# Optimization experiments

Hardware: AMD Instinct MI355X
Metric: run time of the kernel (lower is better)

The kernel has to match this reference:

```python
import jax, jax.numpy as jnp
import numpy as np

WIDTH = 16
N_LAYERS = 2
N_HIGHWAY = 2
B, S, D = 16, 2048, 512


def _causal_band(x, w):
    # out[:, t] = sum_{d=0..WIDTH} w[WIDTH-d] * x[:, t-d]  (x[<0]=0)
    out = w[WIDTH] * x
    for d in range(1, WIDTH + 1):
        out = out + w[WIDTH - d] * jnp.pad(x, ((0, 0), (d, 0), (0, 0)))[:, :S]
    return out


def _anticausal_band(x, w):
    # out[:, t] = sum_{d=0..WIDTH} w[d] * x[:, t+d]  (x[>=S]=0)
    out = w[0] * x
    for d in range(1, WIDTH + 1):
        out = out + w[d] * jnp.pad(x, ((0, 0), (0, d), (0, 0)))[:, d:]
    return out


def _highway(x, Ws, bs):
    # Ws: [N_HIGHWAY, D, 2D], bs: [N_HIGHWAY, 2D] (allennlp Highway, relu activation)
    for i in range(N_HIGHWAY):
        proj = jnp.einsum('bsd,de->bse', x, Ws[i]) + bs[i]
        nonlinear, gate = jnp.split(proj, 2, axis=-1)
        g = jax.nn.sigmoid(gate)
        x = g * x + (1.0 - g) * jax.nn.relu(nonlinear)
    return x


def setup_inputs() -> dict:
    key = jax.random.key(0)
    ks = jax.random.split(key, 8)
    scale = 1.0 / np.sqrt(D)
    return {
        'inputs': jax.random.normal(ks[0], (B, S, D), jnp.float32),
        'masks': jnp.ones((B, S), jnp.int32),
        'fw_band': jax.random.normal(ks[1], (N_LAYERS, WIDTH + 1), jnp.float32),
        'bw_band': jax.random.normal(ks[2], (N_LAYERS, WIDTH + 1), jnp.float32),
        'fw_W': jax.random.normal(ks[3], (N_LAYERS, N_HIGHWAY, D, 2 * D), jnp.float32) * scale,
        'fw_b': jax.random.normal(ks[4], (N_LAYERS, N_HIGHWAY, 2 * D), jnp.float32) * 0.1,
        'bw_W': jax.random.normal(ks[5], (N_LAYERS, N_HIGHWAY, D, 2 * D), jnp.float32) * scale,
        'bw_b': jax.random.normal(ks[6], (N_LAYERS, N_HIGHWAY, 2 * D), jnp.float32) * 0.1,
    }


def reference(inputs, masks, fw_band, bw_band, fw_W, fw_b, bw_W, bw_b):
    fwd = inputs
    bwd = inputs
    outs = []
    for l in range(N_LAYERS):
        fwd = _causal_band(fwd, fw_band[l])
        bwd = _anticausal_band(bwd, bw_band[l])
        fwd = _highway(fwd, fw_W[l], fw_b[l])
        bwd = _highway(bwd, bw_W[l], bw_b[l])
        outs.append(jnp.concatenate([fwd, bwd], axis=-1))
    return jnp.stack(outs, axis=0)  # [N_LAYERS, B, S, 2D]
```

## Files before the change

### kernel.cpp

```cpp
#include <hip/hip_runtime.h>
#include <hip/hip_bf16.h>

#define B_ 16
#define S_ 2048
#define D_ 512
#define M_ (B_ * S_)

typedef __attribute__((ext_vector_type(8))) _Float16 f16x8;
typedef __attribute__((ext_vector_type(4))) float f32x4;

#define GLOAD_LDS16(gp, lp)                                                   \
    __builtin_amdgcn_global_load_lds(                                         \
        (const __attribute__((address_space(1))) unsigned int*)(gp),          \
        (__attribute__((address_space(3))) unsigned int*)(lp), 16, 0, 0)

__global__ __launch_bounds__(256) void prep_w_kernel(
    const float* __restrict__ fwW, const float* __restrict__ bwW,
    _Float16* __restrict__ Wt)
{
    __shared__ float tile[32][33];
    int bid = blockIdx.x;
    int mat = bid >> 9;
    int t   = bid & 511;
    int kt  = t >> 5;
    int nt  = t & 31;
    int l   = mat >> 2;
    int dir = (mat >> 1) & 1;
    int h   = mat & 1;
    const float* src = (dir ? bwW : fwW) + (long long)(l * 2 + h) * (512LL * 1024);

    int tx = threadIdx.x & 31;
    int ty = threadIdx.x >> 5;
#pragma unroll
    for (int j = 0; j < 4; ++j) {
        int k = kt * 32 + ty + j * 8;
        tile[ty + j * 8][tx] = src[(long long)k * 1024 + nt * 32 + tx];
    }
    __syncthreads();
    _Float16* dst = Wt + (long long)mat * (1024LL * 512);
#pragma unroll
    for (int j = 0; j < 4; ++j) {
        int n = nt * 32 + ty + j * 8;
        dst[(long long)n * 512 + kt * 32 + tx] = (_Float16)tile[tx][ty + j * 8];
    }
}

__global__ __launch_bounds__(256) void band_conv_kernel(
    const float* __restrict__ src, long long bstride, int rstride,
    const float* __restrict__ w17, int causal,
    _Float16* __restrict__ Th)
{
    int id = blockIdx.x * 256 + threadIdx.x;
    int c  = id & (D_ - 1);
    int tt = (id >> 9) & (S_ / 4 - 1);
    int b  = id >> 18;
    int t0 = tt * 4;

    float w[17];
#pragma unroll
    for (int e = 0; e < 17; ++e) w[e] = w17[e];

    float buf[20];
    int tbase = t0 - (causal ? 16 : 0);
    const float* sp = src + (long long)b * bstride + c;
#pragma unroll
    for (int i = 0; i < 20; ++i) {
        int t = tbase + i;
        buf[i] = (t >= 0 && t < S_) ? sp[(long long)t * rstride] : 0.f;
    }
#pragma unroll
    for (int j = 0; j < 4; ++j) {
        float a = 0.f;
#pragma unroll
        for (int e = 0; e <= 16; ++e) a = fmaf(w[e], buf[j + e], a);
        Th[((long long)(b * S_ + t0 + j)) * D_ + c] = (_Float16)a;
    }
}

__global__ __launch_bounds__(256) void hw_step_kernel(
    const _Float16* __restrict__ Xh,
    const _Float16* __restrict__ Wt,
    const float* __restrict__ bias,
    float* __restrict__ outF, int outF_stride,
    _Float16* __restrict__ outH)
{
    __shared__ _Float16 As[2 * 128 * 32];
    __shared__ _Float16 Bs[2 * 128 * 32];

    int tid = threadIdx.x;

    int f = blockIdx.x;
    int L = (f & 7) * 256 + (f >> 3);
    int colb = L & 7;
    int rowb = L >> 3;
    long long m0 = (long long)rowb * 128;
    int n0   = colb * 64;

    int lane = tid & 63;
    int wave = tid >> 6;
    int wm   = (wave & 1) * 64;
    int wn   = (wave >> 1) * 32;
    int ln   = lane & 15;
    int q    = lane >> 4;

    f32x4 acc[2][2][4];
#pragma unroll
    for (int h = 0; h < 2; ++h)
#pragma unroll
        for (int jn = 0; jn < 2; ++jn)
#pragma unroll
            for (int i = 0; i < 4; ++i) acc[h][jn][i] = (f32x4){0.f, 0.f, 0.f, 0.f};

    int srow = tid >> 2;
    int scol = (tid & 3) * 8;
    const _Float16* gA0 = Xh + (m0 + srow) * 512 + scol;
    const _Float16* gA1 = gA0 + 64 * 512;
    const _Float16* gB0 = Wt + (long long)(n0 + srow) * 512 + scol;
    const _Float16* gB1 = gB0 + 512 * 512;

    auto stage = [&](int b, int k0) {
        _Float16* lA = &As[b * 4096 + tid * 8];
        _Float16* lB = &Bs[b * 4096 + tid * 8];
        GLOAD_LDS16(gA0 + k0, lA);
        GLOAD_LDS16(gA1 + k0, lA + 64 * 32);
        GLOAD_LDS16(gB0 + k0, lB);
        GLOAD_LDS16(gB1 + k0, lB + 64 * 32);
    };

    auto compute = [&](int b) {
        const _Float16* Ab = &As[b * 4096];
        const _Float16* Bb = &Bs[b * 4096];
        f16x8 af[4];
#pragma unroll
        for (int i = 0; i < 4; ++i)
            af[i] = *(const f16x8*)&Ab[(wm + i * 16 + ln) * 32 + q * 8];
        f16x8 bfr[2][2];
#pragma unroll
        for (int h = 0; h < 2; ++h)
#pragma unroll
            for (int jn = 0; jn < 2; ++jn)
                bfr[h][jn] = *(const f16x8*)&Bb[(h * 64 + wn + jn * 16 + ln) * 32 + q * 8];
#pragma unroll
        for (int h = 0; h < 2; ++h)
#pragma unroll
            for (int jn = 0; jn < 2; ++jn)
#pragma unroll
                for (int i = 0; i < 4; ++i)
                    acc[h][jn][i] = __builtin_amdgcn_mfma_f32_16x16x32_f16(
                        af[i], bfr[h][jn], acc[h][jn][i], 0, 0, 0);
    };

    stage(0, 0);
    __syncthreads();
    int cur = 0;
    for (int k0 = 32; k0 < 512; k0 += 32) {
        stage(cur ^ 1, k0);
        compute(cur);
        __syncthreads();
        cur ^= 1;
    }
    compute(cur);

    __syncthreads();
    {
        int xrow = tid >> 3;
        int xcol = (tid & 7) * 8;
        const _Float16* gx = Xh + (m0 + xrow) * 512 + n0 + xcol;
#pragma unroll
        for (int j = 0; j < 4; ++j)
            GLOAD_LDS16(gx + (long long)j * 32 * 512, &As[j * 2048 + tid * 8]);
    }
    __syncthreads();

#pragma unroll
    for (int jn = 0; jn < 2; ++jn) {
        int c  = n0 + wn + jn * 16 + ln;
        int xc = wn + jn * 16 + ln;
        float bnl = bias[c];
        float bg  = bias[512 + c];
#pragma unroll
        for (int i = 0; i < 4; ++i) {
#pragma unroll
            for (int r = 0; r < 4; ++r) {
                int xr = wm + i * 16 + q * 4 + r;
                long long m = m0 + xr;
                float nl = acc[0][jn][i][r] + bnl;
                float gt = acc[1][jn][i][r] + bg;
                float g  = 1.f / (1.f + __expf(-gt));
                float xv = (float)As[xr * 64 + xc];
                float o  = g * xv + (1.f - g) * fmaxf(nl, 0.f);
                if (outF) outF[m * (long long)outF_stride + c] = o;
                if (outH) outH[m * 512 + c] = (_Float16)o;
            }
        }
    }
}

extern "C" void kernel_launch(void* const* d_in, const int* in_sizes, int n_in,
                              void* d_out, int out_size, void* d_ws, size_t ws_size,
                              hipStream_t stream)
{
    const float* inputs  = (const float*)d_in[0];
    const float* fw_band = (const float*)d_in[2];
    const float* bw_band = (const float*)d_in[3];
    const float* fw_W    = (const float*)d_in[4];
    const float* fw_b    = (const float*)d_in[5];
    const float* bw_W    = (const float*)d_in[6];
    const float* bw_b    = (const float*)d_in[7];
    float* out = (float*)d_out;

    char* ws = (char*)d_ws;
    const size_t SZ_TH = (size_t)M_ * D_ * 2;
    _Float16* Th = (_Float16*)(ws);
    _Float16* Hh = (_Float16*)(ws + SZ_TH);
    _Float16* Wt = (_Float16*)(ws + 2 * SZ_TH);

    prep_w_kernel<<<4096, 256, 0, stream>>>(fw_W, bw_W, Wt);

    for (int l = 0; l < 2; ++l) {
        for (int dir = 0; dir < 2; ++dir) {
            const float* src; long long bstride; int rstride;
            if (l == 0) { src = inputs; bstride = (long long)S_ * D_; rstride = D_; }
            else {
                src = out + (long long)(l - 1) * M_ * 1024 + dir * 512;
                bstride = (long long)S_ * 1024; rstride = 1024;
            }
            const float* band = (dir ? bw_band : fw_band) + l * 17;
            band_conv_kernel<<<(B_ * (S_ / 4) * D_) / 256, 256, 0, stream>>>(
                src, bstride, rstride, band, dir == 0 ? 1 : 0, Th);

            const _Float16* W0 = Wt + (size_t)((l * 2 + dir) * 2 + 0) * (1024 * 512);
            const _Float16* W1 = Wt + (size_t)((l * 2 + dir) * 2 + 1) * (1024 * 512);
            const float* bias = (dir ? bw_b : fw_b) + (size_t)(l * 2) * 1024;

            hw_step_kernel<<<2048, 256, 0, stream>>>(Th, W0, bias, nullptr, 0, Hh);
            float* oF = out + (long long)l * M_ * 1024 + dir * 512;
            hw_step_kernel<<<2048, 256, 0, stream>>>(Hh, W1, bias + 1024, oF, 1024, nullptr);
        }
    }
}
```

Measured before the change: 892.1 us.

## Enlarge highway GEMM tile with swizzled LDS and fine-grained staged pipeline

The highway GEMM kernel moves from a 128x64 output tile (times two for gate and nonlinear halves) with K-step 32 to a 256x128 tile with K-step 64, using 512 threads and a 128KB LDS double buffer. LDS rows get an XOR swizzle to avoid bank conflicts. Global-to-LDS loads are split into per-phase stages interleaved with the MFMA blocks, using explicit vmcnt waits, barriers and s_setprio. The aim is more operand reuse per byte loaded and better overlap of loads with math, at the cost of much higher LDS use, roughly one block per CU, and tricky manual synchronisation.

Result: faster. 821.3 us (-7.9%).

```diff
diff --git a/kernel.cpp b/kernel.cpp
--- a/kernel.cpp
+++ b/kernel.cpp
@@ -77,117 +77,141 @@
     }
 }
 
-__global__ __launch_bounds__(256) void hw_step_kernel(
+__global__ __launch_bounds__(512, 2) void hw_step_kernel(
     const _Float16* __restrict__ Xh,
     const _Float16* __restrict__ Wt,
     const float* __restrict__ bias,
     float* __restrict__ outF, int outF_stride,
     _Float16* __restrict__ outH)
 {
-    __shared__ _Float16 As[2 * 128 * 32];
-    __shared__ _Float16 Bs[2 * 128 * 32];
+    __shared__ _Float16 lds[65536];
+    char* ldsb = (char*)lds;
 
     int tid = threadIdx.x;
 
     int f = blockIdx.x;
-    int L = (f & 7) * 256 + (f >> 3);
-    int colb = L & 7;
-    int rowb = L >> 3;
-    long long m0 = (long long)rowb * 128;
-    int n0   = colb * 64;
+    int L = (f & 7) * 64 + (f >> 3);
+    int colb = L & 3;
+    int rowb = L >> 2;
+    long long m0 = (long long)rowb * 256;
+    int n0 = colb * 128;
 
     int lane = tid & 63;
     int wave = tid >> 6;
-    int wm   = (wave & 1) * 64;
-    int wn   = (wave >> 1) * 32;
-    int ln   = lane & 15;
-    int q    = lane >> 4;
-
-    f32x4 acc[2][2][4];
+    int wave_m = wave >> 1;
+    int wave_n = wave & 1;
+    int wrow = wave_m * 64;
+    int wn   = wave_n * 64;
+    int ln = lane & 15;
+    int q  = lane >> 4;
+
+    int rloc  = tid >> 3;
+    int cperm = 8 * ((tid & 7) ^ (rloc & 7));
+    const _Float16* gA  = Xh + (m0 + rloc) * 512 + cperm;
+    const _Float16* gBn = Wt + (long long)(n0 + rloc) * 512 + cperm;
+    const _Float16* gBg = Wt + (long long)(512 + n0 + rloc) * 512 + cperm;
+
+    auto stageA = [&](int b, int kt, int h2) {
+#pragma unroll
+        for (int j = 0; j < 2; ++j)
+            GLOAD_LDS16(gA + (long long)(h2 * 128 + j * 64) * 512 + kt * 64,
+                        ldsb + b * 32768 + h2 * 16384 + (j * 512 + tid) * 16);
+    };
+    auto stageB = [&](int b, int kt, int h2) {
+        const _Float16* g = h2 ? gBg : gBn;
+#pragma unroll
+        for (int j = 0; j < 2; ++j)
+            GLOAD_LDS16(g + (long long)(j * 64) * 512 + kt * 64,
+                        ldsb + 65536 + b * 32768 + h2 * 16384 + (j * 512 + tid) * 16);
+    };
+
+    f32x4 acc[2][4][4];
 #pragma unroll
     for (int h = 0; h < 2; ++h)
 #pragma unroll
-        for (int jn = 0; jn < 2; ++jn)
+        for (int jn = 0; jn < 4; ++jn)
 #pragma unroll
             for (int i = 0; i < 4; ++i) acc[h][jn][i] = (f32x4){0.f, 0.f, 0.f, 0.f};
 
-    int srow = tid >> 2;
-    int scol = (tid & 3) * 8;
-    const _Float16* gA0 = Xh + (m0 + srow) * 512 + scol;
-    const _Float16* gA1 = gA0 + 64 * 512;
-    const _Float16* gB0 = Wt + (long long)(n0 + srow) * 512 + scol;
-    const _Float16* gB1 = gB0 + 512 * 512;
-
-    auto stage = [&](int b, int k0) {
-        _Float16* lA = &As[b * 4096 + tid * 8];
-        _Float16* lB = &Bs[b * 4096 + tid * 8];
-        GLOAD_LDS16(gA0 + k0, lA);
-        GLOAD_LDS16(gA1 + k0, lA + 64 * 32);
-        GLOAD_LDS16(gB0 + k0, lB);
-        GLOAD_LDS16(gB1 + k0, lB + 64 * 32);
-    };
-
-    auto compute = [&](int b) {
-        const _Float16* Ab = &As[b * 4096];
-        const _Float16* Bb = &Bs[b * 4096];
-        f16x8 af[4];
-#pragma unroll
-        for (int i = 0; i < 4; ++i)
-            af[i] = *(const f16x8*)&Ab[(wm + i * 16 + ln) * 32 + q * 8];
-        f16x8 bfr[2][2];
-#pragma unroll
-        for (int h = 0; h < 2; ++h)
-#pragma unroll
-            for (int jn = 0; jn < 2; ++jn)
-                bfr[h][jn] = *(const f16x8*)&Bb[(h * 64 + wn + jn * 16 + ln) * 32 + q * 8];
-#pragma unroll
-        for (int h = 0; h < 2; ++h)
-#pragma unroll
-            for (int jn = 0; jn < 2; ++jn)
+    stageB(0, 0, 0);
+    stageA(0, 0, 0);
+    stageA(0, 0, 1);
+    stageB(0, 0, 1);
+    stageB(1, 1, 0);
+    asm volatile("s_waitcnt vmcnt(2)" ::: "memory");
+    __builtin_amdgcn_s_barrier();
+
+    f16x8 af[4];
+    for (int kt = 0; kt < 8; ++kt) {
+        int b = kt & 1;
+        const char* Ab = ldsb + b * 32768;
+        const char* Bb = ldsb + 65536 + b * 32768;
+#pragma unroll
+        for (int p = 0; p < 4; ++p) {
+            const int h = p & 1, ks = p >> 1;
+            const int cb = ks * 64 + q * 16;
+            if ((p & 1) == 0) {
+#pragma unroll
+                for (int i = 0; i < 4; ++i) {
+                    int row = wrow + i * 16 + ln;
+                    af[i] = *(const f16x8*)(Ab + row * 128 + (cb ^ ((row & 7) << 4)));
+                }
+            }
+            f16x8 bf[4];
+#pragma unroll
+            for (int jn = 0; jn < 4; ++jn) {
+                int row = h * 128 + wn + jn * 16 + ln;
+                bf[jn] = *(const f16x8*)(Bb + row * 128 + (cb ^ ((row & 7) << 4)));
+            }
+            if (p == 0) { if (kt + 1 < 8) stageA(b ^ 1, kt + 1, 0); }
+            if (p == 1) { if (kt + 1 < 8) stageA(b ^ 1, kt + 1, 1); }
+            if (p == 2) { if (kt + 1 < 8) stageB(b ^ 1, kt + 1, 1); }
+            if (p == 3) {
+                if (kt + 2 < 8) stageB(b, kt + 2, 0);
+                if (kt < 6)       asm volatile("s_waitcnt vmcnt(2)" ::: "memory");
+                else if (kt == 6) asm volatile("s_waitcnt vmcnt(0)" ::: "memory");
+            }
+            __builtin_amdgcn_s_barrier();
+            asm volatile("s_waitcnt lgkmcnt(0)" ::: "memory");
+            __builtin_amdgcn_sched_barrier(0);
+            __builtin_amdgcn_s_setprio(1);
+#pragma unroll
+            for (int jn = 0; jn < 4; ++jn)
 #pragma unroll
                 for (int i = 0; i < 4; ++i)
                     acc[h][jn][i] = __builtin_amdgcn_mfma_f32_16x16x32_f16(
-                        af[i], bfr[h][jn], acc[h][jn][i], 0, 0, 0);
-    };
-
-    stage(0, 0);
-    __syncthreads();
-    int cur = 0;
-    for (int k0 = 32; k0 < 512; k0 += 32) {
-        stage(cur ^ 1, k0);
-        compute(cur);
-        __syncthreads();
-        cur ^= 1;
-    }
-    compute(cur);
-
-    __syncthreads();
-    {
-        int xrow = tid >> 3;
-        int xcol = (tid & 7) * 8;
-        const _Float16* gx = Xh + (m0 + xrow) * 512 + n0 + xcol;
-#pragma unroll
-        for (int j = 0; j < 4; ++j)
-            GLOAD_LDS16(gx + (long long)j * 32 * 512, &As[j * 2048 + tid * 8]);
-    }
-    __syncthreads();
-
-#pragma unroll
-    for (int jn = 0; jn < 2; ++jn) {
-        int c  = n0 + wn + jn * 16 + ln;
-        int xc = wn + jn * 16 + ln;
+                        af[i], bf[jn], acc[h][jn][i], 0, 0, 0);
+            __builtin_amdgcn_s_setprio(0);
+            __builtin_amdgcn_s_barrier();
+        }
+    }
+
+#pragma unroll
+    for (int j = 0; j < 8; ++j) {
+        int idx = j * 512 + tid;
+        int row = idx >> 4;
+        int col = (idx & 15) * 8;
+        GLOAD_LDS16(Xh + (m0 + row) * 512 + n0 + col, ldsb + idx * 16);
+    }
+    asm volatile("s_waitcnt vmcnt(0)" ::: "memory");
+    __builtin_amdgcn_s_barrier();
+
+#pragma unroll
+    for (int jn = 0; jn < 4; ++jn) {
+        int oc = wn + jn * 16 + ln;
+        int c  = n0 + oc;
         float bnl = bias[c];
         float bg  = bias[512 + c];
 #pragma unroll
         for (int i = 0; i < 4; ++i) {
 #pragma unroll
             for (int r = 0; r < 4; ++r) {
-                int xr = wm + i * 16 + q * 4 + r;
+                int xr = wrow + i * 16 + q * 4 + r;
                 long long m = m0 + xr;
                 float nl = acc[0][jn][i][r] + bnl;
                 float gt = acc[1][jn][i][r] + bg;
                 float g  = 1.f / (1.f + __expf(-gt));
-                float xv = (float)As[xr * 64 + xc];
+                float xv = (float)lds[xr * 128 + oc];
                 float o  = g * xv + (1.f - g) * fmaxf(nl, 0.f);
                 if (outF) outF[m * (long long)outF_stride + c] = o;
                 if (outH) outH[m * 512 + c] = (_Float16)o;
@@ -233,9 +257,9 @@
             const _Float16* W1 = Wt + (size_t)((l * 2 + dir) * 2 + 1) * (1024 * 512);
             const float* bias = (dir ? bw_b : fw_b) + (size_t)(l * 2) * 1024;
 
-            hw_step_kernel<<<2048, 256, 0, stream>>>(Th, W0, bias, nullptr, 0, Hh);
+            hw_step_kernel<<<512, 512, 0, stream>>>(Th, W0, bias, nullptr, 0, Hh);
             float* oF = out + (long long)l * M_ * 1024 + dir * 512;
-            hw_step_kernel<<<2048, 256, 0, stream>>>(Hh, W1, bias + 1024, oF, 1024, nullptr);
+            hw_step_kernel<<<512, 512, 0, stream>>>(Hh, W1, bias + 1024, oF, 1024, nullptr);
         }
     }
 }
```
